# Optimization experiments

Measured on AMD Instinct MI355X. Metric: run time of the kernel, lower is better.

The kernel has to match this reference:

```python
import jax, jax.numpy as jnp
import numpy as np
import math

D_MODEL = 1024
N_HEAD = 16
HEAD_DIM = D_MODEL // N_HEAD


def setup_inputs() -> dict:
    key = jax.random.key(0)
    ks = jax.random.split(key, 9)
    B, S = 2, 2048
    x = jax.random.normal(ks[0], (B, S, D_MODEL), dtype=jnp.float32)
    # nn.Linear weights are [out, in]; default-ish init scale 0.02, phase projs std=0.005
    w = lambda k, std: jax.random.normal(k, (D_MODEL, D_MODEL), dtype=jnp.float32) * std
    return {
        "x": x,
        "Wq_amp": w(ks[1], 0.02),
        "Wk_amp": w(ks[2], 0.02),
        "Wq_phi": w(ks[3], 0.005),
        "Wk_phi": w(ks[4], 0.005),
        "Wv": w(ks[5], 0.02),
        "Wo": w(ks[6], 0.02),
        "score_log_scale": jnp.zeros((N_HEAD,), dtype=jnp.float32),
    }


def _split_heads(t):
    B, S, _ = t.shape
    return t.reshape(B, S, N_HEAD, HEAD_DIM).transpose(0, 2, 1, 3)  # [B,H,S,hd]


def reference(x, Wq_amp, Wk_amp, Wq_phi, Wk_phi, Wv, Wo, score_log_scale):
    B, S, _ = x.shape
    eps = 1e-6
    # amplitude (softplus) and phase (pi * tanh) projections
    q_amp = _split_heads(jax.nn.softplus(x @ Wq_amp.T))
    k_amp = _split_heads(jax.nn.softplus(x @ Wk_amp.T))
    q_phi = _split_heads(math.pi * jnp.tanh(x @ Wq_phi.T))
    k_phi = _split_heads(math.pi * jnp.tanh(x @ Wk_phi.T))
    # RMS-normalize amplitudes over head_dim
    q_amp = q_amp / jnp.sqrt(jnp.mean(q_amp * q_amp, axis=-1, keepdims=True) + eps)
    k_amp = k_amp / jnp.sqrt(jnp.mean(k_amp * k_amp, axis=-1, keepdims=True) + eps)
    # interference components
    q_cos = q_amp * jnp.cos(q_phi)
    q_sin = q_amp * jnp.sin(q_phi)
    k_cos = k_amp * jnp.cos(k_phi)
    k_sin = k_amp * jnp.sin(k_phi)
    # two-term score matmul, scaled
    scores = (jnp.einsum("bhqd,bhkd->bhqk", q_cos, k_cos)
              + jnp.einsum("bhqd,bhkd->bhqk", q_sin, k_sin)) / math.sqrt(HEAD_DIM)
    scores = scores * jnp.exp(score_log_scale)[None, :, None, None]
    # causal mask + softmax
    mask = jnp.tril(jnp.ones((S, S), dtype=bool))
    scores = jnp.where(mask[None, None], scores, -jnp.inf)
    attn = jax.nn.softmax(scores, axis=-1)
    v = _split_heads(x @ Wv.T)
    out = jnp.einsum("bhqk,bhkd->bhqd", attn, v)
    out = out.transpose(0, 2, 1, 3).reshape(B, S, D_MODEL)
    return out @ Wo.T
```

## Files before the change

### kernel.cpp

```cpp
#include <hip/hip_runtime.h>
#include <hip/hip_bf16.h>
#include <math.h>

#define S_LEN 2048
#define NH 16
#define HD 64
#define DM 1024
#define NTOK 4096
#define NBH 32

typedef __attribute__((ext_vector_type(8))) __bf16 bf16x8;
typedef __attribute__((ext_vector_type(8))) ushort ushort8;
typedef __attribute__((ext_vector_type(4))) ushort ushort4v;
typedef __attribute__((ext_vector_type(4))) float f32x4;
typedef __attribute__((ext_vector_type(16))) float f32x16;
typedef __attribute__((ext_vector_type(4))) uint u32x4;

__device__ __forceinline__ ushort f2b(float x) {
  __hip_bfloat16 h = __float2bfloat16(x);
  return *reinterpret_cast<ushort*>(&h);
}

__device__ __forceinline__ uint pk2(float lo, float hi) {
  return (uint)f2b(lo) | ((uint)f2b(hi) << 16);
}

__device__ __forceinline__ void gload16b(const void* g, void* l) {
  __builtin_amdgcn_global_load_lds((const __attribute__((address_space(1))) void*)g,
                                   (__attribute__((address_space(3))) void*)l, 16, 0, 0);
}

#define MFMA16(a, b, c) __builtin_amdgcn_mfma_f32_16x16x32_bf16((a), (b), (c), 0, 0, 0)
#define MFMA32(a, b, c) __builtin_amdgcn_mfma_f32_32x32x16_bf16((a), (b), (c), 0, 0, 0)

struct CvtArgs {
  const float* src[7];
  ushort* dst[7];
  int n[7];
};

__global__ void cvt_kernel(CvtArgs a) {
  int arr = blockIdx.y;
  long i = ((long)blockIdx.x * blockDim.x + threadIdx.x) * 8;
  if (i >= a.n[arr]) return;
  const float* s = a.src[arr];
  ushort* d = a.dst[arr];
  float4 v0 = *reinterpret_cast<const float4*>(s + i);
  float4 v1 = *reinterpret_cast<const float4*>(s + i + 4);
  ushort8 r;
  r[0] = f2b(v0.x); r[1] = f2b(v0.y); r[2] = f2b(v0.z); r[3] = f2b(v0.w);
  r[4] = f2b(v1.x); r[5] = f2b(v1.y); r[6] = f2b(v1.z); r[7] = f2b(v1.w);
  *reinterpret_cast<ushort8*>(d + i) = r;
}

__global__ __launch_bounds__(256, 2) void qkproj_kernel(
    const ushort* __restrict__ A,
    const ushort* __restrict__ Wqa, const ushort* __restrict__ Wqp,
    const ushort* __restrict__ Wka, const ushort* __restrict__ Wkp,
    const ushort* __restrict__ Wv, const float* __restrict__ sls,
    ushort* __restrict__ qext, ushort* __restrict__ kext, ushort* __restrict__ vT) {
  __shared__ __align__(16) ushort Alds[3][4096];
  __shared__ __align__(16) ushort B0lds[3][4096];
  __shared__ __align__(16) ushort B1lds[3][4096];
  const int d = blockIdx.x;
  const int xc = d & 7, c = d >> 3;
  const int u = (c < 64) ? (xc * 64 + c) : (512 + xc * 32 + (c - 64));
  int z, bx, by;
  if (u < 512) { z = u >> 8; int v = u & 255; bx = v & 7; by = v >> 3; }
  else         { z = 2;      int v = u - 512; bx = v & 7; by = v >> 3; }
  const int t = threadIdx.x;
  const int lane = t & 63;
  const int wave = t >> 6;
  const int wm = wave >> 1, wn = wave & 1;
  const int l15 = lane & 15, g = lane >> 4;
  const int mbase = by * 128, nbase = bx * 128;
  const int K = DM;
  const int srow = t >> 2;
  const int sx = (srow >> 1) & 3;
  const int scol = (((t & 3) ^ sx)) * 8;
  const int xr = (l15 >> 1) & 3;
  const ushort* Ag = A + (size_t)(mbase + srow) * K + scol;
  const ushort* Wa = (z == 0) ? Wqa : (z == 1) ? Wka : Wv;
  const ushort* Wp = (z == 0) ? Wqp : Wkp;
  const ushort* Wag = Wa + (size_t)(nbase + srow) * K + scol;
  const ushort* Wpg = (z < 2) ? (Wp + (size_t)(nbase + srow) * K + scol) : Wag;

  const int nk = K / 32;
  f32x4 accA[4][4] = {};

  if (z < 2) {
    f32x4 accP[4][4] = {};
    auto stage = [&](int buf, int kt) {
      gload16b(Ag + kt, &Alds[buf][t * 8]);
      gload16b(Ag + kt + (size_t)64 * K, &Alds[buf][t * 8 + 64 * 32]);
      gload16b(Wag + kt, &B0lds[buf][t * 8]);
      gload16b(Wag + kt + (size_t)64 * K, &B0lds[buf][t * 8 + 64 * 32]);
      gload16b(Wpg + kt, &B1lds[buf][t * 8]);
      gload16b(Wpg + kt + (size_t)64 * K, &B1lds[buf][t * 8 + 64 * 32]);
    };
    stage(0, 0);
    stage(1, 32);
    int cur = 0;
    for (int kt = 0; kt < nk; ++kt) {
      if (kt + 2 < nk) {
        int b2 = cur + 2; if (b2 >= 3) b2 -= 3;
        stage(b2, (kt + 2) * 32);
        asm volatile("s_waitcnt vmcnt(12)" ::: "memory");
      } else if (kt + 1 < nk) {
        asm volatile("s_waitcnt vmcnt(6)" ::: "memory");
      } else {
        asm volatile("s_waitcnt vmcnt(0)" ::: "memory");
      }
      __builtin_amdgcn_s_barrier();
      bf16x8 af[4], ba[4], bp[4];
#pragma unroll
      for (int i = 0; i < 4; i++)
        af[i] = *reinterpret_cast<const bf16x8*>(
            &Alds[cur][(wm * 64 + i * 16 + l15) * 32 + (g ^ xr) * 8]);
#pragma unroll
      for (int j = 0; j < 4; j++) {
        ba[j] = *reinterpret_cast<const bf16x8*>(
            &B0lds[cur][(wn * 64 + j * 16 + l15) * 32 + (g ^ xr) * 8]);
        bp[j] = *reinterpret_cast<const bf16x8*>(
            &B1lds[cur][(wn * 64 + j * 16 + l15) * 32 + (g ^ xr) * 8]);
      }
      __builtin_amdgcn_s_setprio(1);
#pragma unroll
      for (int i = 0; i < 4; i++)
#pragma unroll
        for (int j = 0; j < 4; j++) {
          accA[i][j] = MFMA16(af[i], ba[j], accA[i][j]);
          accP[i][j] = MFMA16(af[i], bp[j], accP[i][j]);
        }
      __builtin_amdgcn_s_setprio(0);
      __builtin_amdgcn_s_barrier();
      cur = (cur + 1 == 3) ? 0 : cur + 1;
    }
    const int row0 = mbase + wm * 64;
    const int h = (nbase >> 6) + wn;
    const float scale = (z == 0) ? __expf(sls[h]) * 0.125f : 1.0f;
    ushort* ext = (z == 0) ? qext : kext;
#pragma unroll
    for (int i = 0; i < 4; i++) {
#pragma unroll
      for (int r = 0; r < 4; r++) {
        float sp[4];
        float ss = 0.0f;
#pragma unroll
        for (int j = 0; j < 4; j++) {
          float v = accA[i][j][r];
          sp[j] = fmaxf(v, 0.0f) + __logf(1.0f + __expf(-fabsf(v)));
          ss += sp[j] * sp[j];
        }
        ss += __shfl_xor(ss, 1);
        ss += __shfl_xor(ss, 2);
        ss += __shfl_xor(ss, 4);
        ss += __shfl_xor(ss, 8);
        float rn = rsqrtf(ss * (1.0f / 64.0f) + 1e-6f) * scale;
        const int token = row0 + i * 16 + g * 4 + r;
        const int bb = token >> 11, sidx = token & 2047;
        ushort* base = ext + (((size_t)(bb * NH + h) * S_LEN + sidx) << 7);
#pragma unroll
        for (int j = 0; j < 4; j++) {
          float e = __expf(2.0f * accP[i][j][r]);
          float th = 1.0f - 2.0f * __builtin_amdgcn_rcpf(e + 1.0f);
          float phi = 3.14159265358979f * th;
          float sn = __sinf(phi), cs = __cosf(phi);
          float a = sp[j] * rn;
          int dd = j * 16 + l15;
          base[dd] = f2b(a * cs);
          base[64 + dd] = f2b(a * sn);
        }
      }
    }
  } else {
    auto stage = [&](int buf, int kt) {
      gload16b(Ag + kt, &Alds[buf][t * 8]);
      gload16b(Ag + kt + (size_t)64 * K, &Alds[buf][t * 8 + 64 * 32]);
      gload16b(Wag + kt, &B0lds[buf][t * 8]);
      gload16b(Wag + kt + (size_t)64 * K, &B0lds[buf][t * 8 + 64 * 32]);
    };
    stage(0, 0);
    stage(1, 32);
    int cur = 0;
    for (int kt = 0; kt < nk; ++kt) {
      if (kt + 2 < nk) {
        int b2 = cur + 2; if (b2 >= 3) b2 -= 3;
        stage(b2, (kt + 2) * 32);
        asm volatile("s_waitcnt vmcnt(8)" ::: "memory");
      } else if (kt + 1 < nk) {
        asm volatile("s_waitcnt vmcnt(4)" ::: "memory");
      } else {
        asm volatile("s_waitcnt vmcnt(0)" ::: "memory");
      }
      __builtin_amdgcn_s_barrier();
      bf16x8 af[4], ba[4];
#pragma unroll
      for (int i = 0; i < 4; i++)
        af[i] = *reinterpret_cast<const bf16x8*>(
            &Alds[cur][(wm * 64 + i * 16 + l15) * 32 + (g ^ xr) * 8]);
#pragma unroll
      for (int j = 0; j < 4; j++)
        ba[j] = *reinterpret_cast<const bf16x8*>(
            &B0lds[cur][(wn * 64 + j * 16 + l15) * 32 + (g ^ xr) * 8]);
      __builtin_amdgcn_s_setprio(1);
#pragma unroll
      for (int i = 0; i < 4; i++)
#pragma unroll
        for (int j = 0; j < 4; j++)
          accA[i][j] = MFMA16(af[i], ba[j], accA[i][j]);
      __builtin_amdgcn_s_setprio(0);
      __builtin_amdgcn_s_barrier();
      cur = (cur + 1 == 3) ? 0 : cur + 1;
    }
    const int row0 = mbase + wm * 64, col0 = nbase + wn * 64;
#pragma unroll
    for (int i = 0; i < 4; i++)
#pragma unroll
      for (int j = 0; j < 4; j++) {
        int col = col0 + j * 16 + l15;
        int h = col >> 6, hd = col & 63;
        int t0 = row0 + i * 16 + g * 4;
        int bb = t0 >> 11, s0 = t0 & 2047;
        ushort4v w;
#pragma unroll
        for (int r = 0; r < 4; r++) w[r] = f2b(accA[i][j][r]);
        *reinterpret_cast<ushort4v*>(
            &vT[(((size_t)(bb * NH + h) * HD + hd) << 11) + s0]) = w;
      }
  }
}

__global__ __launch_bounds__(256) void gemm_bt(const ushort* __restrict__ A,
                                               const ushort* __restrict__ W,
                                               float* __restrict__ Cout,
                                               int M, int N, int K) {
  __shared__ __align__(16) ushort Alds[4][4096];
  __shared__ __align__(16) ushort Blds[4][4096];
  const int d = blockIdx.x;
  const int u = (d & 7) * 32 + (d >> 3);
  const int bx = u & 7, by = u >> 3;
  const int t = threadIdx.x;
  const int lane = t & 63;
  const int wave = t >> 6;
  const int wm = wave >> 1, wn = wave & 1;
  const int l15 = lane & 15, g = lane >> 4;
  const int mbase = by * 128, nbase = bx * 128;
  const int srow = t >> 2;
  const int sx = (srow >> 1) & 3;
  const int scol = (((t & 3) ^ sx)) * 8;
  const int xr = (l15 >> 1) & 3;
  const ushort* Ag = A + (size_t)(mbase + srow) * K + scol;
  const ushort* Wg = W + (size_t)(nbase + srow) * K + scol;
  auto stage = [&](int buf, int kt) {
    gload16b(Ag + kt, &Alds[buf][t * 8]);
    gload16b(Ag + kt + (size_t)64 * K, &Alds[buf][t * 8 + 64 * 32]);
    gload16b(Wg + kt, &Blds[buf][t * 8]);
    gload16b(Wg + kt + (size_t)64 * K, &Blds[buf][t * 8 + 64 * 32]);
  };
  const int nk = K / 32;
  stage(0, 0);
  stage(1, 32);
  stage(2, 64);
  f32x4 acc[4][4] = {};
  for (int kt = 0; kt < nk; ++kt) {
    const int cur = kt & 3;
    if (kt + 3 < nk) {
      stage((cur + 3) & 3, (kt + 3) * 32);
      asm volatile("s_waitcnt vmcnt(12)" ::: "memory");
    } else if (kt + 2 < nk) {
      asm volatile("s_waitcnt vmcnt(8)" ::: "memory");
    } else if (kt + 1 < nk) {
      asm volatile("s_waitcnt vmcnt(4)" ::: "memory");
    } else {
      asm volatile("s_waitcnt vmcnt(0)" ::: "memory");
    }
    __builtin_amdgcn_s_barrier();
    bf16x8 af[4], bfr[4];
#pragma unroll
    for (int i = 0; i < 4; i++)
      af[i] = *reinterpret_cast<const bf16x8*>(
          &Alds[cur][(wm * 64 + i * 16 + l15) * 32 + (g ^ xr) * 8]);
#pragma unroll
    for (int j = 0; j < 4; j++)
      bfr[j] = *reinterpret_cast<const bf16x8*>(
          &Blds[cur][(wn * 64 + j * 16 + l15) * 32 + (g ^ xr) * 8]);
    __builtin_amdgcn_s_setprio(1);
#pragma unroll
    for (int i = 0; i < 4; i++)
#pragma unroll
      for (int j = 0; j < 4; j++)
        acc[i][j] = MFMA16(af[i], bfr[j], acc[i][j]);
    __builtin_amdgcn_s_setprio(0);
    __builtin_amdgcn_s_barrier();
  }
  const int row0 = mbase + wm * 64, col0 = nbase + wn * 64;
#pragma unroll
  for (int i = 0; i < 4; i++)
#pragma unroll
    for (int j = 0; j < 4; j++)
#pragma unroll
      for (int r = 0; r < 4; r++) {
        int row = row0 + i * 16 + g * 4 + r;
        int col = col0 + j * 16 + l15;
        Cout[(size_t)row * N + col] = acc[i][j][r];
      }
}

__device__ __forceinline__ void stage_kv(const char* Kp, const char* Vp, int kb,
                                         char* buf, int wave, int lane) {
#pragma unroll
  for (int c = 0; c < 4; c++) {
    int i = wave * 4 + c;
    int kvl = i * 4 + (lane >> 4);
    int slot = (lane & 15) ^ (kvl & 7);
    gload16b(Kp + (size_t)(kb + kvl) * 256 + slot * 16, buf + i * 1024);
  }
#pragma unroll
  for (int c = 0; c < 2; c++) {
    int i = wave * 2 + c;
    int hd = i * 8 + (lane >> 3);
    int slot = (lane & 7) ^ (hd & 7);
    gload16b(Vp + (size_t)hd * (S_LEN * 2) + (size_t)kb * 2 + slot * 16,
             buf + 16384 + i * 1024);
  }
}

__global__ __launch_bounds__(256, 2) void attn_kernel(const ushort* __restrict__ qext,
                                                      const ushort* __restrict__ kext,
                                                      const ushort* __restrict__ vT,
                                                      ushort* __restrict__ attnout) {
  __shared__ __align__(16) char lds[2][24576];
  const int u = blockIdx.x;
  const int uh = u >> 8, v = u & 255;
  const int bh = v >> 3, j = v & 7;
  const int qt = uh ? (15 - j) : j;
  const int b = bh >> 4, h = bh & 15;
  const int wave = threadIdx.x >> 6, lane = threadIdx.x & 63;
  const int l31 = lane & 31, hi = lane >> 5;
  const int qb = qt * 128;
  const int qw = qb + wave * 32;
  const int qa = qw + l31;
  const char* Kp = (const char*)(kext + (size_t)bh * S_LEN * 128);
  const char* Vp = (const char*)(vT + (size_t)bh * HD * S_LEN);
  const ushort* Qp = qext + (size_t)bh * S_LEN * 128;
  const int nt = 2 * qt + 2;
  const int ksw = l31 & 7;

  stage_kv(Kp, Vp, 0, lds[0], wave, lane);
  bf16x8 qf[8];
#pragma unroll
  for (int s = 0; s < 8; s++)
    qf[s] = *reinterpret_cast<const bf16x8*>(&Qp[(size_t)qa * 128 + s * 16 + hi * 8]);

  f32x16 o0 = {}, o1 = {};
  float m = -1e30f, ls = 0.0f;

  for (int t = 0; t < nt; ++t) {
    const int cur = t & 1;
    const int kb = t << 6;
    if (t + 1 < nt) {
      stage_kv(Kp, Vp, (t + 1) << 6, lds[cur ^ 1], wave, lane);
      asm volatile("s_waitcnt vmcnt(6)" ::: "memory");
    } else {
      asm volatile("s_waitcnt vmcnt(0)" ::: "memory");
    }
    __builtin_amdgcn_s_barrier();

    const char* Kb = lds[cur];
    const char* Vb = lds[cur] + 16384;

    f32x16 st0 = {}, st1 = {};
    __builtin_amdgcn_s_setprio(1);
#pragma unroll
    for (int s = 0; s < 8; s++) {
      int sl = ((s * 2 + hi) ^ ksw) << 4;
      bf16x8 k0 = *(const bf16x8*)(Kb + l31 * 256 + sl);
      bf16x8 k1 = *(const bf16x8*)(Kb + (32 + l31) * 256 + sl);
      st0 = MFMA32(k0, qf[s], st0);
      st1 = MFMA32(k1, qf[s], st1);
    }
    __builtin_amdgcn_s_setprio(0);

    if (kb + 64 > qw) {
#pragma unroll
      for (int r = 0; r < 16; r++) {
        int kv = kb + (r & 3) + 8 * (r >> 2) + 4 * hi;
        if (kv > qa) st0[r] = -1e30f;
        if (kv + 32 > qa) st1[r] = -1e30f;
      }
    }
    float pm = -1e30f;
#pragma unroll
    for (int r = 0; r < 16; r++) pm = fmaxf(pm, fmaxf(st0[r], st1[r]));
    pm = fmaxf(pm, __shfl_xor(pm, 32));
    if (!__all(pm <= m + 8.0f)) {
      float mn = fmaxf(m, pm);
      float corr = __expf(m - mn);
      m = mn;
      ls *= corr;
#pragma unroll
      for (int r = 0; r < 16; r++) { o0[r] *= corr; o1[r] *= corr; }
    }
    float ssum = 0.0f;
#pragma unroll
    for (int r = 0; r < 16; r++) {
      st0[r] = __expf(st0[r] - m);
      st1[r] = __expf(st1[r] - m);
      ssum += st0[r] + st1[r];
    }
    ssum += __shfl_xor(ssum, 32);
    ls += ssum;

    u32x4 pb[4];
#pragma unroll
    for (int half = 0; half < 2; half++) {
      const f32x16& st = half ? st1 : st0;
      uint cA0 = pk2(st[0], st[1]),  cA1 = pk2(st[2], st[3]);
      uint cB0 = pk2(st[4], st[5]),  cB1 = pk2(st[6], st[7]);
      uint cC0 = pk2(st[8], st[9]),  cC1 = pk2(st[10], st[11]);
      uint cD0 = pk2(st[12], st[13]), cD1 = pk2(st[14], st[15]);
      uint xA0 = __shfl_xor(cA0, 32), xA1 = __shfl_xor(cA1, 32);
      uint xB0 = __shfl_xor(cB0, 32), xB1 = __shfl_xor(cB1, 32);
      uint xC0 = __shfl_xor(cC0, 32), xC1 = __shfl_xor(cC1, 32);
      uint xD0 = __shfl_xor(cD0, 32), xD1 = __shfl_xor(cD1, 32);
      u32x4 lo, hi4;
      lo[0] = cA0; lo[1] = cA1; lo[2] = xA0; lo[3] = xA1;
      hi4[0] = xB0; hi4[1] = xB1; hi4[2] = cB0; hi4[3] = cB1;
      pb[half * 2] = hi ? hi4 : lo;
      u32x4 lo2, hi2;
      lo2[0] = cC0; lo2[1] = cC1; lo2[2] = xC0; lo2[3] = xC1;
      hi2[0] = xD0; hi2[1] = xD1; hi2[2] = cD0; hi2[3] = cD1;
      pb[half * 2 + 1] = hi ? hi2 : lo2;
    }
    __builtin_amdgcn_s_setprio(1);
#pragma unroll
    for (int ks = 0; ks < 4; ks++) {
      int sl = ((ks * 2 + hi) ^ ksw) << 4;
      bf16x8 v0 = *(const bf16x8*)(Vb + l31 * 128 + sl);
      bf16x8 v1 = *(const bf16x8*)(Vb + (32 + l31) * 128 + sl);
      bf16x8 pbb = *reinterpret_cast<const bf16x8*>(&pb[ks]);
      o0 = MFMA32(v0, pbb, o0);
      o1 = MFMA32(v1, pbb, o1);
    }
    __builtin_amdgcn_s_setprio(0);
    __builtin_amdgcn_s_barrier();
  }

  float inv = 1.0f / ls;
  ushort* Op = attnout + ((size_t)b * S_LEN + qa) * DM + h * HD;
#pragma unroll
  for (int g4 = 0; g4 < 4; g4++) {
    ushort4v w0, w1;
#pragma unroll
    for (int jj = 0; jj < 4; jj++) {
      w0[jj] = f2b(o0[4 * g4 + jj] * inv);
      w1[jj] = f2b(o1[4 * g4 + jj] * inv);
    }
    *reinterpret_cast<ushort4v*>(Op + 8 * g4 + 4 * hi) = w0;
    *reinterpret_cast<ushort4v*>(Op + 32 + 8 * g4 + 4 * hi) = w1;
  }
}

extern "C" void kernel_launch(void* const* d_in, const int* in_sizes, int n_in,
                              void* d_out, int out_size, void* d_ws, size_t ws_size,
                              hipStream_t stream) {
  const float* x   = (const float*)d_in[0];
  const float* Wqa = (const float*)d_in[1];
  const float* Wka = (const float*)d_in[2];
  const float* Wqp = (const float*)d_in[3];
  const float* Wkp = (const float*)d_in[4];
  const float* Wv  = (const float*)d_in[5];
  const float* Wo  = (const float*)d_in[6];
  const float* sls = (const float*)d_in[7];

  char* ws = (char*)d_ws;
  ushort* x_bf = (ushort*)ws; ws += (size_t)NTOK * DM * 2;
  ushort* w_bf[6];
  for (int i = 0; i < 6; i++) { w_bf[i] = (ushort*)ws; ws += (size_t)DM * DM * 2; }
  ushort* qext = (ushort*)ws; ws += (size_t)NBH * S_LEN * 128 * 2;
  ushort* kext = (ushort*)ws; ws += (size_t)NBH * S_LEN * 128 * 2;
  ushort* vT   = (ushort*)ws; ws += (size_t)NBH * HD * S_LEN * 2;
  ushort* attn = (ushort*)ws; ws += (size_t)NTOK * DM * 2;

  CvtArgs ca;
  ca.src[0] = x; ca.dst[0] = x_bf; ca.n[0] = NTOK * DM;
  const float* wsrc[6] = {Wqa, Wka, Wqp, Wkp, Wv, Wo};
  for (int i = 0; i < 6; i++) { ca.src[i + 1] = wsrc[i]; ca.dst[i + 1] = w_bf[i]; ca.n[i + 1] = DM * DM; }
  dim3 cg((NTOK * DM / 8 + 255) / 256, 7);
  hipLaunchKernelGGL(cvt_kernel, cg, dim3(256), 0, stream, ca);

  hipLaunchKernelGGL(qkproj_kernel, dim3(768), dim3(256), 0, stream,
                     x_bf, w_bf[0], w_bf[2], w_bf[1], w_bf[3], w_bf[4], sls,
                     qext, kext, vT);

  hipLaunchKernelGGL(attn_kernel, dim3(512), dim3(256), 0, stream,
                     qext, kext, vT, attn);

  hipLaunchKernelGGL(gemm_bt, dim3(256), dim3(256), 0, stream, attn, w_bf[5],
                     (float*)d_out, NTOK, DM, DM);
}
```

Measured before the change: 156.8 us.

## Split long causal query tiles across two blocks with a merge kernel

The attention kernel now runs 768 blocks. The lower 8 query tiles are processed whole, and each of the upper 8 tiles is split into two KV ranges whose partial outputs, max and sum go to an fp32 scratch buffer. A new merge kernel combines each pair with log-sum-exp rescaling. The block-to-head mapping also groups heads by XCD for L2 locality, and launch bounds are raised to 3 waves per SIMD. This balances causal work and adds parallelism, at the cost of an extra launch and scratch traffic, and it may increase register pressure.

```diff
diff --git a/kernel.cpp b/kernel.cpp
--- a/kernel.cpp
+++ b/kernel.cpp
@@ -326,15 +326,24 @@
   }
 }
 
-__global__ __launch_bounds__(256, 2) void attn_kernel(const ushort* __restrict__ qext,
+__global__ __launch_bounds__(256, 3) void attn_kernel(const ushort* __restrict__ qext,
                                                       const ushort* __restrict__ kext,
                                                       const ushort* __restrict__ vT,
-                                                      ushort* __restrict__ attnout) {
+                                                      ushort* __restrict__ attnout,
+                                                      float* __restrict__ part) {
   __shared__ __align__(16) char lds[2][24576];
-  const int u = blockIdx.x;
-  const int uh = u >> 8, v = u & 255;
-  const int bh = v >> 3, j = v & 7;
-  const int qt = uh ? (15 - j) : j;
+  const int d = blockIdx.x;
+  const int xcd = d & 7, c = d >> 3;
+  const int bh = xcd * 4 + (c & 3);
+  const int w = c >> 2;
+  int qt, t0, t1, half;
+  bool split;
+  if (w < 8) { qt = w; t0 = 0; t1 = 2 * qt + 1; split = false; half = 0; }
+  else {
+    int ww = w - 8;
+    qt = 8 + (ww >> 1); half = ww & 1; split = true;
+    if (half == 0) { t0 = 0; t1 = qt; } else { t0 = qt + 1; t1 = 2 * qt + 1; }
+  }
   const int b = bh >> 4, h = bh & 15;
   const int wave = threadIdx.x >> 6, lane = threadIdx.x & 63;
   const int l31 = lane & 31, hi = lane >> 5;
@@ -344,10 +353,9 @@
   const char* Kp = (const char*)(kext + (size_t)bh * S_LEN * 128);
   const char* Vp = (const char*)(vT + (size_t)bh * HD * S_LEN);
   const ushort* Qp = qext + (size_t)bh * S_LEN * 128;
-  const int nt = 2 * qt + 2;
   const int ksw = l31 & 7;
 
-  stage_kv(Kp, Vp, 0, lds[0], wave, lane);
+  stage_kv(Kp, Vp, t0 << 6, lds[0], wave, lane);
   bf16x8 qf[8];
 #pragma unroll
   for (int s = 0; s < 8; s++)
@@ -356,10 +364,10 @@
   f32x16 o0 = {}, o1 = {};
   float m = -1e30f, ls = 0.0f;
 
-  for (int t = 0; t < nt; ++t) {
-    const int cur = t & 1;
+  for (int t = t0; t <= t1; ++t) {
+    const int cur = (t - t0) & 1;
     const int kb = t << 6;
-    if (t + 1 < nt) {
+    if (t < t1) {
       stage_kv(Kp, Vp, (t + 1) << 6, lds[cur ^ 1], wave, lane);
       asm volatile("s_waitcnt vmcnt(6)" ::: "memory");
     } else {
@@ -414,8 +422,8 @@
 
     u32x4 pb[4];
 #pragma unroll
-    for (int half = 0; half < 2; half++) {
-      const f32x16& st = half ? st1 : st0;
+    for (int hf = 0; hf < 2; hf++) {
+      const f32x16& st = hf ? st1 : st0;
       uint cA0 = pk2(st[0], st[1]),  cA1 = pk2(st[2], st[3]);
       uint cB0 = pk2(st[4], st[5]),  cB1 = pk2(st[6], st[7]);
       uint cC0 = pk2(st[8], st[9]),  cC1 = pk2(st[10], st[11]);
@@ -427,11 +435,11 @@
       u32x4 lo, hi4;
       lo[0] = cA0; lo[1] = cA1; lo[2] = xA0; lo[3] = xA1;
       hi4[0] = xB0; hi4[1] = xB1; hi4[2] = cB0; hi4[3] = cB1;
-      pb[half * 2] = hi ? hi4 : lo;
+      pb[hf * 2] = hi ? hi4 : lo;
       u32x4 lo2, hi2;
       lo2[0] = cC0; lo2[1] = cC1; lo2[2] = xC0; lo2[3] = xC1;
       hi2[0] = xD0; hi2[1] = xD1; hi2[2] = cD0; hi2[3] = cD1;
-      pb[half * 2 + 1] = hi ? hi2 : lo2;
+      pb[hf * 2 + 1] = hi ? hi2 : lo2;
     }
     __builtin_amdgcn_s_setprio(1);
 #pragma unroll
@@ -447,18 +455,57 @@
     __builtin_amdgcn_s_barrier();
   }
 
-  float inv = 1.0f / ls;
-  ushort* Op = attnout + ((size_t)b * S_LEN + qa) * DM + h * HD;
-#pragma unroll
-  for (int g4 = 0; g4 < 4; g4++) {
-    ushort4v w0, w1;
-#pragma unroll
-    for (int jj = 0; jj < 4; jj++) {
-      w0[jj] = f2b(o0[4 * g4 + jj] * inv);
-      w1[jj] = f2b(o1[4 * g4 + jj] * inv);
-    }
-    *reinterpret_cast<ushort4v*>(Op + 8 * g4 + 4 * hi) = w0;
-    *reinterpret_cast<ushort4v*>(Op + 32 + 8 * g4 + 4 * hi) = w1;
+  if (!split) {
+    float inv = 1.0f / ls;
+    ushort* Op = attnout + ((size_t)b * S_LEN + qa) * DM + h * HD;
+#pragma unroll
+    for (int g4 = 0; g4 < 4; g4++) {
+      ushort4v w0, w1;
+#pragma unroll
+      for (int jj = 0; jj < 4; jj++) {
+        w0[jj] = f2b(o0[4 * g4 + jj] * inv);
+        w1[jj] = f2b(o1[4 * g4 + jj] * inv);
+      }
+      *reinterpret_cast<ushort4v*>(Op + 8 * g4 + 4 * hi) = w0;
+      *reinterpret_cast<ushort4v*>(Op + 32 + 8 * g4 + 4 * hi) = w1;
+    }
+  } else {
+    float* P = part + ((size_t)(half * 256 + bh * 8 + (qt - 8)) * 128
+                       + (wave * 32 + l31)) * 72;
+#pragma unroll
+    for (int g4 = 0; g4 < 4; g4++) {
+      float4 a0 = make_float4(o0[4 * g4], o0[4 * g4 + 1], o0[4 * g4 + 2], o0[4 * g4 + 3]);
+      float4 a1 = make_float4(o1[4 * g4], o1[4 * g4 + 1], o1[4 * g4 + 2], o1[4 * g4 + 3]);
+      *reinterpret_cast<float4*>(P + 8 * g4 + 4 * hi) = a0;
+      *reinterpret_cast<float4*>(P + 32 + 8 * g4 + 4 * hi) = a1;
+    }
+    if (hi == 0) { P[64] = m; P[65] = ls; }
+  }
+}
+
+__global__ void attn_merge(const float* __restrict__ part, ushort* __restrict__ attnout) {
+  const int blk = blockIdx.x;
+  const int row = threadIdx.x;
+  const int bh = blk >> 3, qt = (blk & 7) + 8;
+  const float* Pa = part + ((size_t)blk * 128 + row) * 72;
+  const float* Pb = part + ((size_t)(256 + blk) * 128 + row) * 72;
+  float mA = Pa[64], lsA = Pa[65], mB = Pb[64], lsB = Pb[65];
+  float M = fmaxf(mA, mB);
+  float ca = __expf(mA - M), cb = __expf(mB - M);
+  float inv = 1.0f / (lsA * ca + lsB * cb);
+  const int b = bh >> 4, h = bh & 15;
+  const int q = qt * 128 + row;
+  ushort* Op = attnout + ((size_t)b * S_LEN + q) * DM + h * HD;
+#pragma unroll
+  for (int dd = 0; dd < 64; dd += 4) {
+    float4 va = *reinterpret_cast<const float4*>(Pa + dd);
+    float4 vb = *reinterpret_cast<const float4*>(Pb + dd);
+    ushort4v wv;
+    wv[0] = f2b((va.x * ca + vb.x * cb) * inv);
+    wv[1] = f2b((va.y * ca + vb.y * cb) * inv);
+    wv[2] = f2b((va.z * ca + vb.z * cb) * inv);
+    wv[3] = f2b((va.w * ca + vb.w * cb) * inv);
+    *reinterpret_cast<ushort4v*>(Op + dd) = wv;
   }
 }
 
@@ -482,6 +529,7 @@
   ushort* kext = (ushort*)ws; ws += (size_t)NBH * S_LEN * 128 * 2;
   ushort* vT   = (ushort*)ws; ws += (size_t)NBH * HD * S_LEN * 2;
   ushort* attn = (ushort*)ws; ws += (size_t)NTOK * DM * 2;
+  float* part  = (float*)ws;  ws += (size_t)2 * 256 * 128 * 72 * 4;
 
   CvtArgs ca;
   ca.src[0] = x; ca.dst[0] = x_bf; ca.n[0] = NTOK * DM;
@@ -494,8 +542,9 @@
                      x_bf, w_bf[0], w_bf[2], w_bf[1], w_bf[3], w_bf[4], sls,
                      qext, kext, vT);
 
-  hipLaunchKernelGGL(attn_kernel, dim3(512), dim3(256), 0, stream,
-                     qext, kext, vT, attn);
+  hipLaunchKernelGGL(attn_kernel, dim3(768), dim3(256), 0, stream,
+                     qext, kext, vT, attn, part);
+  hipLaunchKernelGGL(attn_merge, dim3(256), dim3(128), 0, stream, part, attn);
 
   hipLaunchKernelGGL(gemm_bt, dim3(256), dim3(256), 0, stream, attn, w_bf[5],
                      (float*)d_out, NTOK, DM, DM);
```

New measurement: 155.9 us. About the same (-0.6%).
